# Kernel tuning notes

Measured on AMD Instinct MI355X. Metric: run time of the kernel, lower is better.

## Reference

```python
import jax, jax.numpy as jnp
import numpy as np
import math

N = 50000
E = 500000
IN_C = 128
T_FEAT = 16
OUT_C = 128
EPS = 1e-5
NEG_SLOPE = 0.01


def setup_inputs() -> dict:
    key = jax.random.key(0)
    ks = jax.random.split(key, 10)
    x = jax.random.normal(ks[0], (N, IN_C), dtype=jnp.float32)
    edge_index = jax.random.randint(ks[1], (2, E), 0, N, dtype=jnp.int64)
    edge_weight = jax.random.uniform(ks[2], (E,), dtype=jnp.float32)
    time_diff = jax.random.uniform(ks[3], (1,), dtype=jnp.float32)
    d_in = IN_C + T_FEAT
    morning_freq = jax.random.normal(ks[4], (T_FEAT,), dtype=jnp.float32)
    W_gcn = jax.random.normal(ks[5], (d_in, OUT_C), dtype=jnp.float32) / np.sqrt(d_in)
    b_gcn = jnp.zeros((OUT_C,), dtype=jnp.float32)
    gamma = jnp.ones((OUT_C,), dtype=jnp.float32)
    beta = jnp.zeros((OUT_C,), dtype=jnp.float32)
    W_lin = jax.random.normal(ks[6], (OUT_C, OUT_C), dtype=jnp.float32) / np.sqrt(OUT_C)
    b_lin = jax.random.normal(ks[7], (OUT_C,), dtype=jnp.float32) * 0.01
    return {"x": x, "edge_index": edge_index, "edge_weight": edge_weight,
            "time_diff": time_diff, "morning_freq": morning_freq,
            "W_gcn": W_gcn, "b_gcn": b_gcn, "gamma": gamma, "beta": beta,
            "W_lin": W_lin, "b_lin": b_lin}


def _gcn_conv(h, edge_index, edge_weight):
    # PyG GCNConv aggregation: add self-loops (weight 1), symmetric normalization.
    row, col = edge_index[0], edge_index[1]
    loop = jnp.arange(N, dtype=edge_index.dtype)
    row_f = jnp.concatenate([row, loop])
    col_f = jnp.concatenate([col, loop])
    ew_f = jnp.concatenate([edge_weight, jnp.ones((N,), dtype=h.dtype)])
    deg = jax.ops.segment_sum(ew_f, col_f, num_segments=N)
    dinv = jnp.where(deg > 0, jax.lax.rsqrt(jnp.maximum(deg, 1e-12)), 0.0)
    norm = dinv[row_f] * ew_f * dinv[col_f]                 # [E+N]
    msg = h[row_f] * norm[:, None]                          # gather + scale
    return jax.ops.segment_sum(msg, col_f, num_segments=N)  # scatter-add


def reference(x, edge_index, edge_weight, time_diff, morning_freq,
              W_gcn, b_gcn, gamma, beta, W_lin, b_lin):
    td = time_diff[0]
    # time_segment == 'morning_peak': sin encoding, tiled over all nodes
    enc = jnp.sin(td * morning_freq * math.pi)              # [T]
    enc = jnp.broadcast_to(enc[None, :], (x.shape[0], T_FEAT))
    h = jnp.concatenate([x, enc], axis=1)                   # [N, in+T]
    h = h @ W_gcn                                           # GCN linear transform
    h = _gcn_conv(h, edge_index, edge_weight) + b_gcn       # [N, out]
    # BatchNorm1d (training-mode batch statistics, biased variance)
    mean = jnp.mean(h, axis=0)
    var = jnp.mean(jnp.square(h - mean), axis=0)
    h = gamma * (h - mean) * jax.lax.rsqrt(var + EPS) + beta
    h = jnp.where(h >= 0, h, NEG_SLOPE * h)                 # LeakyReLU
    h = h @ W_lin + b_lin                                   # Linear (dropout=eval identity)
    return h
```

## Files before the change

### kernel.cpp

```cpp
#include <hip/hip_runtime.h>
#include <hip/hip_bf16.h>

#define NN 50000
#define NE 500000
#define C 128
#define NBLK ((NN + 255) / 256)
#define HISTB ((NE + 255) / 256)
#define SPB2 (NN / 16)
#define RB 128
#define RROWS ((SPB2 + RB - 1) / RB)
#define GB ((NN + 63) / 64)
#define BN_EPS 1e-5f
#define NEG 0.01f
#define WSCALE 16777216.0f
#define WMASK  0xFFFFFFFFFFFULL

typedef __attribute__((ext_vector_type(8))) short bf16x8;
typedef __attribute__((ext_vector_type(4))) float f32x4;
typedef unsigned long long ull;

__device__ inline unsigned short f2bf(float f) {
    unsigned int u = __float_as_uint(f);
    unsigned int r = (u + 0x7fffu + ((u >> 16) & 1u)) >> 16;
    return (unsigned short)r;
}
__device__ inline unsigned int pack2(float a, float b) {
    return (unsigned int)f2bf(a) | ((unsigned int)f2bf(b) << 16);
}
__device__ inline float4 bf4_to_f4(unsigned int lo, unsigned int hi) {
    float4 r;
    r.x = __uint_as_float(lo << 16);
    r.y = __uint_as_float(lo & 0xffff0000u);
    r.z = __uint_as_float(hi << 16);
    r.w = __uint_as_float(hi & 0xffff0000u);
    return r;
}

__global__ __launch_bounds__(256) void setup_kernel(const float* __restrict__ Wg,
                                                    const float* __restrict__ Wl,
                                                    unsigned int* __restrict__ Wgt,
                                                    unsigned int* __restrict__ Wlt,
                                                    const float* __restrict__ td,
                                                    const float* __restrict__ mf,
                                                    float* __restrict__ cvec,
                                                    float* __restrict__ zreg) {
    const int b = blockIdx.x;
    const int t = threadIdx.x;
    if (b < 128) {
        long i = (long)b * 256 + t;
        const long n = 2L * NN + 516;
        const long s = 128L * 256;
        for (; i < n; i += s) zreg[i] = 0.f;
    } else if (b == 128) {
        const int col = t >> 1;
        const int half = t & 1;
        for (int j = 0; j < 32; j++) {
            int ku = half * 32 + j;
            int k0 = 2 * ku;
            unsigned int g = (unsigned int)((ku >> 2) ^ (col & 15));
            unsigned int slot = (unsigned int)col * 64u + (g << 2) + (unsigned int)(ku & 3);
            Wgt[slot] = pack2(Wg[(size_t)k0 * C + col], Wg[(size_t)(k0 + 1) * C + col]);
            Wlt[slot] = pack2(Wl[(size_t)k0 * C + col], Wl[(size_t)(k0 + 1) * C + col]);
        }
    } else {
        if (t < 128) {
            float tv = td[0];
            float acc = 0.f;
#pragma unroll
            for (int j = 0; j < 16; j++) {
                float s = sinf(tv * mf[j] * 3.14159265358979323846f);
                acc = fmaf(s, Wg[(128 + j) * C + t], acc);
            }
            cvec[t] = acc;
        }
    }
}

__global__ void hist_kernel(const int* __restrict__ ei, const float* __restrict__ ew,
                            ull* __restrict__ hist, int* __restrict__ rank) {
    int e = blockIdx.x * blockDim.x + threadIdx.x;
    if (e < NE) {
        int c = ei[NE + e];
        ull pack = (1ULL << 44) | (ull)(ew[e] * WSCALE);
        ull old = atomicAdd(&hist[c], pack);
        rank[e] = (int)(old >> 44);
    }
}

__global__ __launch_bounds__(256) void gemm1_kernel(const float* __restrict__ X,
                                                    const unsigned int* __restrict__ Wt,
                                                    const float* __restrict__ cvec,
                                                    unsigned short* __restrict__ Hb) {
    __shared__ unsigned int wsh[8192];
    const int t = threadIdx.x;
#pragma unroll
    for (int i = 0; i < 8; i++)
        ((uint4*)wsh)[t + i * 256] = ((const uint4*)Wt)[t + i * 256];

    const int lane = t & 63;
    const int wid = t >> 6;
    const int lrow = lane & 15;
    const int kb = lane >> 4;
    const int row = blockIdx.x * 64 + wid * 16 + lrow;
    const float* xrow = X + (size_t)min(row, NN - 1) * C;

    f32x4 acc[8];
#pragma unroll
    for (int n = 0; n < 8; n++) acc[n] = (f32x4){0.f, 0.f, 0.f, 0.f};
    __syncthreads();

#pragma unroll
    for (int ks = 0; ks < 4; ks++) {
        float4 a0 = *(const float4*)(xrow + ks * 32 + kb * 8);
        float4 a1 = *(const float4*)(xrow + ks * 32 + kb * 8 + 4);
        union { unsigned int u[4]; bf16x8 v; } af;
        af.u[0] = pack2(a0.x, a0.y); af.u[1] = pack2(a0.z, a0.w);
        af.u[2] = pack2(a1.x, a1.y); af.u[3] = pack2(a1.z, a1.w);
        const unsigned int gp = (unsigned int)((ks * 4 + kb) ^ lrow);
#pragma unroll
        for (int n = 0; n < 8; n++) {
            int col = n * 16 + lrow;
            union { uint4 q; bf16x8 v; } bfm;
            bfm.q = *(const uint4*)&wsh[col * 64 + gp * 4];
            acc[n] = __builtin_amdgcn_mfma_f32_16x16x32_bf16(af.v, bfm.v, acc[n], 0, 0, 0);
        }
    }
    const int orow = blockIdx.x * 64 + wid * 16 + kb * 4;
#pragma unroll
    for (int n = 0; n < 8; n++) {
        int col = n * 16 + lrow;
        float cv = cvec[col];
#pragma unroll
        for (int i = 0; i < 4; i++) {
            int r = orow + i;
            if (r < NN) Hb[(size_t)r * C + col] = f2bf(acc[n][i] + cv);
        }
    }
}

__global__ __launch_bounds__(256) void scan_kernel(const ull* __restrict__ hist,
                                                   int* __restrict__ rptr,
                                                   float* __restrict__ dinv,
                                                   ull* __restrict__ bflag) {
    __shared__ int s[256];
    __shared__ int pre[256];
    const int t = threadIdx.x;
    const int b = blockIdx.x;
    const int i = b * 256 + t;
    ull hv = (i < NN) ? hist[i] : 0ULL;
    int v = (int)(hv >> 44);
    s[t] = v;
    __syncthreads();
    for (int off = 1; off < 256; off <<= 1) {
        int add = (t >= off) ? s[t - off] : 0;
        __syncthreads();
        s[t] += add;
        __syncthreads();
    }
    if (t == 255)
        __hip_atomic_store(&bflag[b], (1ULL << 32) | (ull)(unsigned int)s[255],
                           __ATOMIC_RELEASE, __HIP_MEMORY_SCOPE_AGENT);
    int pv = 0;
    if (t < b) {
        ull f;
        do {
            f = __hip_atomic_load(&bflag[t], __ATOMIC_ACQUIRE, __HIP_MEMORY_SCOPE_AGENT);
        } while (!(f >> 32));
        pv = (int)(unsigned int)f;
    }
    pre[t] = pv;
    __syncthreads();
    for (int off = 128; off > 0; off >>= 1) {
        if (t < off) pre[t] += pre[t + off];
        __syncthreads();
    }
    const int boff = pre[0];
    if (i < NN) {
        rptr[i] = boff + s[t] - v;
        float degw = (float)(hv & WMASK) * (1.0f / WSCALE);
        dinv[i] = rsqrtf(degw + 1.0f);
    }
    if (b == 0 && t == 0) rptr[NN] = NE;
}

__global__ void fill_kernel(const int* __restrict__ ei, const float* __restrict__ ew,
                            const float* __restrict__ dinv, const int* __restrict__ rptr,
                            const int* __restrict__ rank, int2* __restrict__ csr) {
    int e = blockIdx.x * blockDim.x + threadIdx.x;
    if (e >= NE) return;
    int r = ei[e], c = ei[NE + e];
    int slot = rptr[c] + rank[e];
    float w = dinv[r] * ew[e] * dinv[c];
    csr[slot] = make_int2(r, __float_as_int(w));
}

__global__ __launch_bounds__(256) void spmm_kernel(const int* __restrict__ rptr,
                                                   const int2* __restrict__ csr,
                                                   const unsigned short* __restrict__ Hb,
                                                   const float* __restrict__ dinv,
                                                   const float* __restrict__ bg,
                                                   unsigned short* __restrict__ H2,
                                                   float* __restrict__ P) {
    const int t = threadIdx.x;
    const int nl = t >> 4;
    const int lane = t & 15;
    const int node = blockIdx.x * 16 + nl;
    const int ch = lane * 8;
    const int s = rptr[node], e = rptr[node + 1];
    const float d = dinv[node];
    const float dd = d * d;
    uint4 hu = *(const uint4*)(Hb + (size_t)node * C + ch);
    float4 hA = bf4_to_f4(hu.x, hu.y), hB = bf4_to_f4(hu.z, hu.w);
    float4 aA = make_float4(dd * hA.x, dd * hA.y, dd * hA.z, dd * hA.w);
    float4 aB = make_float4(dd * hB.x, dd * hB.y, dd * hB.z, dd * hB.w);
    float4 bA = make_float4(0.f, 0.f, 0.f, 0.f);
    float4 bB = make_float4(0.f, 0.f, 0.f, 0.f);
    int j = s;
    for (; j + 4 <= e; j += 4) {
        int2 m0 = csr[j], m1 = csr[j + 1], m2 = csr[j + 2], m3 = csr[j + 3];
        uint4 u0 = *(const uint4*)(Hb + (size_t)m0.x * C + ch);
        uint4 u1 = *(const uint4*)(Hb + (size_t)m1.x * C + ch);
        uint4 u2 = *(const uint4*)(Hb + (size_t)m2.x * C + ch);
        uint4 u3 = *(const uint4*)(Hb + (size_t)m3.x * C + ch);
        float w0 = __int_as_float(m0.y), w1 = __int_as_float(m1.y);
        float w2 = __int_as_float(m2.y), w3 = __int_as_float(m3.y);
        float4 vA, vB;
        vA = bf4_to_f4(u0.x, u0.y); vB = bf4_to_f4(u0.z, u0.w);
        aA.x = fmaf(vA.x, w0, aA.x); aA.y = fmaf(vA.y, w0, aA.y);
        aA.z = fmaf(vA.z, w0, aA.z); aA.w = fmaf(vA.w, w0, aA.w);
        aB.x = fmaf(vB.x, w0, aB.x); aB.y = fmaf(vB.y, w0, aB.y);
        aB.z = fmaf(vB.z, w0, aB.z); aB.w = fmaf(vB.w, w0, aB.w);
        vA = bf4_to_f4(u1.x, u1.y); vB = bf4_to_f4(u1.z, u1.w);
        bA.x = fmaf(vA.x, w1, bA.x); bA.y = fmaf(vA.y, w1, bA.y);
        bA.z = fmaf(vA.z, w1, bA.z); bA.w = fmaf(vA.w, w1, bA.w);
        bB.x = fmaf(vB.x, w1, bB.x); bB.y = fmaf(vB.y, w1, bB.y);
        bB.z = fmaf(vB.z, w1, bB.z); bB.w = fmaf(vB.w, w1, bB.w);
        vA = bf4_to_f4(u2.x, u2.y); vB = bf4_to_f4(u2.z, u2.w);
        aA.x = fmaf(vA.x, w2, aA.x); aA.y = fmaf(vA.y, w2, aA.y);
        aA.z = fmaf(vA.z, w2, aA.z); aA.w = fmaf(vA.w, w2, aA.w);
        aB.x = fmaf(vB.x, w2, aB.x); aB.y = fmaf(vB.y, w2, aB.y);
        aB.z = fmaf(vB.z, w2, aB.z); aB.w = fmaf(vB.w, w2, aB.w);
        vA = bf4_to_f4(u3.x, u3.y); vB = bf4_to_f4(u3.z, u3.w);
        bA.x = fmaf(vA.x, w3, bA.x); bA.y = fmaf(vA.y, w3, bA.y);
        bA.z = fmaf(vA.z, w3, bA.z); bA.w = fmaf(vA.w, w3, bA.w);
        bB.x = fmaf(vB.x, w3, bB.x); bB.y = fmaf(vB.y, w3, bB.y);
        bB.z = fmaf(vB.z, w3, bB.z); bB.w = fmaf(vB.w, w3, bB.w);
    }
    for (; j < e; j++) {
        int2 m0 = csr[j];
        uint4 u0 = *(const uint4*)(Hb + (size_t)m0.x * C + ch);
        float w0 = __int_as_float(m0.y);
        float4 vA = bf4_to_f4(u0.x, u0.y), vB = bf4_to_f4(u0.z, u0.w);
        aA.x = fmaf(vA.x, w0, aA.x); aA.y = fmaf(vA.y, w0, aA.y);
        aA.z = fmaf(vA.z, w0, aA.z); aA.w = fmaf(vA.w, w0, aA.w);
        aB.x = fmaf(vB.x, w0, aB.x); aB.y = fmaf(vB.y, w0, aB.y);
        aB.z = fmaf(vB.z, w0, aB.z); aB.w = fmaf(vB.w, w0, aB.w);
    }
    aA.x += bA.x; aA.y += bA.y; aA.z += bA.z; aA.w += bA.w;
    aB.x += bB.x; aB.y += bB.y; aB.z += bB.z; aB.w += bB.w;
    float4 g0 = *(const float4*)(bg + ch);
    float4 g1 = *(const float4*)(bg + ch + 4);
    aA.x += g0.x; aA.y += g0.y; aA.z += g0.z; aA.w += g0.w;
    aB.x += g1.x; aB.y += g1.y; aB.z += g1.z; aB.w += g1.w;
    uint4 ou;
    ou.x = pack2(aA.x, aA.y); ou.y = pack2(aA.z, aA.w);
    ou.z = pack2(aB.x, aB.y); ou.w = pack2(aB.z, aB.w);
    *(uint4*)(H2 + (size_t)node * C + ch) = ou;

    __shared__ float sred[2][16][128];
    *(float4*)&sred[0][nl][ch]     = aA;
    *(float4*)&sred[0][nl][ch + 4] = aB;
    float4 qA = make_float4(aA.x * aA.x, aA.y * aA.y, aA.z * aA.z, aA.w * aA.w);
    float4 qB = make_float4(aB.x * aB.x, aB.y * aB.y, aB.z * aB.z, aB.w * aB.w);
    *(float4*)&sred[1][nl][ch]     = qA;
    *(float4*)&sred[1][nl][ch + 4] = qB;
    __syncthreads();
    const int q = t >> 7, c2 = t & 127;
    float acc = 0.f;
#pragma unroll
    for (int k = 0; k < 16; k++) acc += sred[q][k][c2];
    P[(size_t)blockIdx.x * 256 + t] = acc;
}

__global__ __launch_bounds__(256) void reduce1_kernel(const float* __restrict__ P,
                                                      float* __restrict__ P2,
                                                      unsigned int* __restrict__ cnt,
                                                      const float* __restrict__ gm,
                                                      const float* __restrict__ bt,
                                                      float* __restrict__ sc,
                                                      float* __restrict__ sh) {
    const int c = threadIdx.x;
    const int r0 = blockIdx.x * RROWS;
    const int r1 = min(r0 + RROWS, SPB2);
    float a0 = 0.f, a1 = 0.f, a2 = 0.f, a3 = 0.f;
    int r = r0;
    for (; r + 4 <= r1; r += 4) {
        a0 += P[(size_t)(r + 0) * 256 + c];
        a1 += P[(size_t)(r + 1) * 256 + c];
        a2 += P[(size_t)(r + 2) * 256 + c];
        a3 += P[(size_t)(r + 3) * 256 + c];
    }
    for (; r < r1; r++) a0 += P[(size_t)r * 256 + c];
    P2[(size_t)blockIdx.x * 256 + c] = (a0 + a1) + (a2 + a3);

    __threadfence();
    __shared__ unsigned int done;
    if (c == 0) done = atomicAdd(cnt, 1u);
    __syncthreads();
    if (done == RB - 1) {
        __threadfence();
        if (c < 128) {
            float s0 = 0.f, s1 = 0.f, q0 = 0.f, q1 = 0.f;
            for (int k = 0; k < RB; k += 2) {
                s0 += P2[(size_t)k * 256 + c];
                q0 += P2[(size_t)k * 256 + 128 + c];
                s1 += P2[(size_t)(k + 1) * 256 + c];
                q1 += P2[(size_t)(k + 1) * 256 + 128 + c];
            }
            float ssum = s0 + s1, ssq = q0 + q1;
            float mean = ssum / (float)NN;
            float var = ssq / (float)NN - mean * mean;
            var = fmaxf(var, 0.f);
            float rs = rsqrtf(var + BN_EPS);
            float s = gm[c] * rs;
            sc[c] = s;
            sh[c] = bt[c] - mean * s;
        }
    }
}

__global__ __launch_bounds__(256) void final_kernel(const unsigned short* __restrict__ H2,
                                                    float* __restrict__ OUT,
                                                    const unsigned int* __restrict__ Wt,
                                                    const float* __restrict__ bl,
                                                    const float* __restrict__ sc,
                                                    const float* __restrict__ sh) {
    __shared__ unsigned int wsh[8192];
    const int t = threadIdx.x;
#pragma unroll
    for (int i = 0; i < 8; i++)
        ((uint4*)wsh)[t + i * 256] = ((const uint4*)Wt)[t + i * 256];

    const int lane = t & 63;
    const int wid = t >> 6;
    const int lrow = lane & 15;
    const int kb = lane >> 4;
    const int row = blockIdx.x * 64 + wid * 16 + lrow;
    const unsigned short* hrow = H2 + (size_t)min(row, NN - 1) * C;

    f32x4 acc[8];
#pragma unroll
    for (int n = 0; n < 8; n++) acc[n] = (f32x4){0.f, 0.f, 0.f, 0.f};
    __syncthreads();

#pragma unroll
    for (int ks = 0; ks < 4; ks++) {
        const int k0 = ks * 32 + kb * 8;
        uint4 hu = *(const uint4*)(hrow + k0);
        float4 v0 = bf4_to_f4(hu.x, hu.y);
        float4 v1 = bf4_to_f4(hu.z, hu.w);
        float4 s0 = *(const float4*)(sc + k0);
        float4 s1 = *(const float4*)(sc + k0 + 4);
        float4 h0 = *(const float4*)(sh + k0);
        float4 h1 = *(const float4*)(sh + k0 + 4);
        float a[8];
        a[0] = fmaf(v0.x, s0.x, h0.x); a[1] = fmaf(v0.y, s0.y, h0.y);
        a[2] = fmaf(v0.z, s0.z, h0.z); a[3] = fmaf(v0.w, s0.w, h0.w);
        a[4] = fmaf(v1.x, s1.x, h1.x); a[5] = fmaf(v1.y, s1.y, h1.y);
        a[6] = fmaf(v1.z, s1.z, h1.z); a[7] = fmaf(v1.w, s1.w, h1.w);
#pragma unroll
        for (int i = 0; i < 8; i++) a[i] = a[i] >= 0.f ? a[i] : NEG * a[i];
        union { unsigned int u[4]; bf16x8 v; } af;
        af.u[0] = pack2(a[0], a[1]); af.u[1] = pack2(a[2], a[3]);
        af.u[2] = pack2(a[4], a[5]); af.u[3] = pack2(a[6], a[7]);
        const unsigned int gp = (unsigned int)((ks * 4 + kb) ^ lrow);
#pragma unroll
        for (int n = 0; n < 8; n++) {
            int col = n * 16 + lrow;
            union { uint4 q; bf16x8 v; } bfm;
            bfm.q = *(const uint4*)&wsh[col * 64 + gp * 4];
            acc[n] = __builtin_amdgcn_mfma_f32_16x16x32_bf16(af.v, bfm.v, acc[n], 0, 0, 0);
        }
    }
    const int orow = blockIdx.x * 64 + wid * 16 + kb * 4;
#pragma unroll
    for (int n = 0; n < 8; n++) {
        int col = n * 16 + lrow;
        float blv = bl[col];
#pragma unroll
        for (int i = 0; i < 4; i++) {
            int r = orow + i;
            if (r < NN) OUT[(size_t)r * C + col] = acc[n][i] + blv;
        }
    }
}

extern "C" void kernel_launch(void* const* d_in, const int* in_sizes, int n_in,
                              void* d_out, int out_size, void* d_ws, size_t ws_size,
                              hipStream_t stream) {
    const float* x  = (const float*)d_in[0];
    const int*   ei = (const int*)d_in[1];
    const float* ew = (const float*)d_in[2];
    const float* td = (const float*)d_in[3];
    const float* mf = (const float*)d_in[4];
    const float* Wg = (const float*)d_in[5];
    const float* bg = (const float*)d_in[6];
    const float* gm = (const float*)d_in[7];
    const float* bt = (const float*)d_in[8];
    const float* Wl = (const float*)d_in[9];
    const float* bl = (const float*)d_in[10];
    float* out = (float*)d_out;

    unsigned short* h1b = (unsigned short*)d_ws;
    unsigned short* h2b = h1b + (size_t)NN * C;
    ull*   hist  = (ull*)(h2b + (size_t)NN * C);
    unsigned int* cnt = (unsigned int*)(hist + NN);
    ull*   bflag = (ull*)(cnt + 4);
    float* dinv  = (float*)(bflag + 256);
    float* cvec  = dinv + NN;
    float* sc    = cvec + C;
    float* sh    = sc + C;
    int*   rptr  = (int*)(sh + C);
    int*   rank  = rptr + NN + 8;
    int2*  csr   = (int2*)(rank + NE);
    float* P     = (float*)(csr + NE);
    float* P2    = P + (size_t)SPB2 * 256;
    unsigned int* Wgt = (unsigned int*)(P2 + RB * 256);
    unsigned int* Wlt = Wgt + 8192;

    setup_kernel<<<130, 256, 0, stream>>>(Wg, Wl, Wgt, Wlt, td, mf, cvec, (float*)hist);
    hist_kernel<<<HISTB, 256, 0, stream>>>(ei, ew, hist, rank);
    gemm1_kernel<<<GB, 256, 0, stream>>>(x, Wgt, cvec, h1b);
    scan_kernel<<<NBLK, 256, 0, stream>>>(hist, rptr, dinv, bflag);
    fill_kernel<<<HISTB, 256, 0, stream>>>(ei, ew, dinv, rptr, rank, csr);
    spmm_kernel<<<SPB2, 256, 0, stream>>>(rptr, csr, h1b, dinv, bg, h2b, P);
    reduce1_kernel<<<RB, 256, 0, stream>>>(P, P2, cnt, gm, bt, sc, sh);
    final_kernel<<<GB, 256, 0, stream>>>(h2b, out, Wlt, bl, sc, sh);
}
```

Baseline: 142.7 us.

## Fuse scan and CSR fill into one kernel with a grid barrier

```diff
diff --git a/kernel.cpp b/kernel.cpp
--- a/kernel.cpp
+++ b/kernel.cpp
@@ -48,7 +48,7 @@
     const int t = threadIdx.x;
     if (b < 128) {
         long i = (long)b * 256 + t;
-        const long n = 2L * NN + 516;
+        const long n = 2L * NN + 520;
         const long s = 128L * 256;
         for (; i < n; i += s) zreg[i] = 0.f;
     } else if (b == 128) {
@@ -80,10 +80,11 @@
                             ull* __restrict__ hist, int* __restrict__ rank) {
     int e = blockIdx.x * blockDim.x + threadIdx.x;
     if (e < NE) {
-        int c = ei[NE + e];
-        ull pack = (1ULL << 44) | (ull)(ew[e] * WSCALE);
+        int c = __builtin_nontemporal_load(ei + NE + e);
+        float wv = __builtin_nontemporal_load(ew + e);
+        ull pack = (1ULL << 44) | (ull)(wv * WSCALE);
         ull old = atomicAdd(&hist[c], pack);
-        rank[e] = (int)(old >> 44);
+        __builtin_nontemporal_store((int)(old >> 44), rank + e);
     }
 }
 
@@ -138,60 +139,80 @@
     }
 }
 
-__global__ __launch_bounds__(256) void scan_kernel(const ull* __restrict__ hist,
-                                                   int* __restrict__ rptr,
-                                                   float* __restrict__ dinv,
-                                                   ull* __restrict__ bflag) {
+__global__ __launch_bounds__(256, 8) void scanfill_kernel(const ull* __restrict__ hist,
+                                                          int* __restrict__ rptr,
+                                                          float* __restrict__ dinv,
+                                                          ull* __restrict__ bflag,
+                                                          unsigned int* __restrict__ gbar,
+                                                          const int* __restrict__ ei,
+                                                          const float* __restrict__ ew,
+                                                          const int* __restrict__ rank,
+                                                          int2* __restrict__ csr) {
     __shared__ int s[256];
     __shared__ int pre[256];
     const int t = threadIdx.x;
     const int b = blockIdx.x;
-    const int i = b * 256 + t;
-    ull hv = (i < NN) ? hist[i] : 0ULL;
-    int v = (int)(hv >> 44);
-    s[t] = v;
-    __syncthreads();
-    for (int off = 1; off < 256; off <<= 1) {
-        int add = (t >= off) ? s[t - off] : 0;
+
+    if (b < NBLK) {
+        const int i = b * 256 + t;
+        ull hv = (i < NN) ? hist[i] : 0ULL;
+        int v = (int)(hv >> 44);
+        s[t] = v;
         __syncthreads();
-        s[t] += add;
+        for (int off = 1; off < 256; off <<= 1) {
+            int add = (t >= off) ? s[t - off] : 0;
+            __syncthreads();
+            s[t] += add;
+            __syncthreads();
+        }
+        if (t == 255)
+            __hip_atomic_store(&bflag[b], (1ULL << 32) | (ull)(unsigned int)s[255],
+                               __ATOMIC_RELEASE, __HIP_MEMORY_SCOPE_AGENT);
+        int pv = 0;
+        if (t < b) {
+            ull f;
+            do {
+                f = __hip_atomic_load(&bflag[t], __ATOMIC_ACQUIRE, __HIP_MEMORY_SCOPE_AGENT);
+            } while (!(f >> 32));
+            pv = (int)(unsigned int)f;
+        }
+        pre[t] = pv;
         __syncthreads();
-    }
-    if (t == 255)
-        __hip_atomic_store(&bflag[b], (1ULL << 32) | (ull)(unsigned int)s[255],
-                           __ATOMIC_RELEASE, __HIP_MEMORY_SCOPE_AGENT);
-    int pv = 0;
-    if (t < b) {
-        ull f;
+        for (int off = 128; off > 0; off >>= 1) {
+            if (t < off) pre[t] += pre[t + off];
+            __syncthreads();
+        }
+        const int boff = pre[0];
+        if (i < NN) {
+            rptr[i] = boff + s[t] - v;
+            float degw = (float)(hv & WMASK) * (1.0f / WSCALE);
+            dinv[i] = rsqrtf(degw + 1.0f);
+        }
+        if (b == 0 && t == 0) rptr[NN] = NE;
+    }
+
+    __threadfence();
+    __syncthreads();
+    if (t == 0) {
+        __hip_atomic_fetch_add(gbar, 1u, __ATOMIC_ACQ_REL, __HIP_MEMORY_SCOPE_AGENT);
+        unsigned int v;
         do {
-            f = __hip_atomic_load(&bflag[t], __ATOMIC_ACQUIRE, __HIP_MEMORY_SCOPE_AGENT);
-        } while (!(f >> 32));
-        pv = (int)(unsigned int)f;
-    }
-    pre[t] = pv;
-    __syncthreads();
-    for (int off = 128; off > 0; off >>= 1) {
-        if (t < off) pre[t] += pre[t + off];
-        __syncthreads();
-    }
-    const int boff = pre[0];
-    if (i < NN) {
-        rptr[i] = boff + s[t] - v;
-        float degw = (float)(hv & WMASK) * (1.0f / WSCALE);
-        dinv[i] = rsqrtf(degw + 1.0f);
-    }
-    if (b == 0 && t == 0) rptr[NN] = NE;
-}
-
-__global__ void fill_kernel(const int* __restrict__ ei, const float* __restrict__ ew,
-                            const float* __restrict__ dinv, const int* __restrict__ rptr,
-                            const int* __restrict__ rank, int2* __restrict__ csr) {
-    int e = blockIdx.x * blockDim.x + threadIdx.x;
-    if (e >= NE) return;
-    int r = ei[e], c = ei[NE + e];
-    int slot = rptr[c] + rank[e];
-    float w = dinv[r] * ew[e] * dinv[c];
-    csr[slot] = make_int2(r, __float_as_int(w));
+            v = __hip_atomic_load(gbar, __ATOMIC_ACQUIRE, __HIP_MEMORY_SCOPE_AGENT);
+        } while (v < (unsigned int)HISTB);
+    }
+    __syncthreads();
+    __threadfence();
+
+    int e = b * 256 + t;
+    if (e < NE) {
+        int r = __builtin_nontemporal_load(ei + e);
+        int c = __builtin_nontemporal_load(ei + NE + e);
+        float wv = __builtin_nontemporal_load(ew + e);
+        int slot = rptr[c] + rank[e];
+        float w = dinv[r] * wv * dinv[c];
+        ull pk = (ull)(unsigned int)r | ((ull)__float_as_uint(w) << 32);
+        __builtin_nontemporal_store(pk, (ull*)(csr + slot));
+    }
 }
 
 __global__ __launch_bounds__(256) void spmm_kernel(const int* __restrict__ rptr,
@@ -416,7 +437,8 @@
     ull*   hist  = (ull*)(h2b + (size_t)NN * C);
     unsigned int* cnt = (unsigned int*)(hist + NN);
     ull*   bflag = (ull*)(cnt + 4);
-    float* dinv  = (float*)(bflag + 256);
+    unsigned int* gbar = (unsigned int*)(bflag + 256);
+    float* dinv  = (float*)(gbar + 4);
     float* cvec  = dinv + NN;
     float* sc    = cvec + C;
     float* sh    = sc + C;
@@ -431,8 +453,7 @@
     setup_kernel<<<130, 256, 0, stream>>>(Wg, Wl, Wgt, Wlt, td, mf, cvec, (float*)hist);
     hist_kernel<<<HISTB, 256, 0, stream>>>(ei, ew, hist, rank);
     gemm1_kernel<<<GB, 256, 0, stream>>>(x, Wgt, cvec, h1b);
-    scan_kernel<<<NBLK, 256, 0, stream>>>(hist, rptr, dinv, bflag);
-    fill_kernel<<<HISTB, 256, 0, stream>>>(ei, ew, dinv, rptr, rank, csr);
+    scanfill_kernel<<<HISTB, 256, 0, stream>>>(hist, rptr, dinv, bflag, gbar, ei, ew, rank, csr);
     spmm_kernel<<<SPB2, 256, 0, stream>>>(rptr, csr, h1b, dinv, bg, h2b, P);
     reduce1_kernel<<<RB, 256, 0, stream>>>(P, P2, cnt, gm, bt, sc, sh);
     final_kernel<<<GB, 256, 0, stream>>>(h2b, out, Wlt, bl, sc, sh);
```

After: 547.2 us. 3.83x slower.
